# Performance work log

Hardware: AMD Instinct MI355X
Metric: run time of the kernel (lower is better)

The kernel has to match this reference:

```python
import jax, jax.numpy as jnp
import numpy as np

V = 1_000_000   # num_embeddings
D = 64          # embedding_dim
B = 16_384      # number of bags (batch)
L = 50          # history length per bag


def setup_inputs() -> dict:
    key = jax.random.key(0)
    k_w, k_i = jax.random.split(key)
    weight = jax.random.normal(k_w, (V, D), dtype=jnp.float32) * 0.01
    indices = jax.random.randint(k_i, (B * L,), 0, V, dtype=jnp.int64)
    # bag start offsets (uniform bags of length L, starting at 0, sorted)
    offsets = (jnp.arange(B, dtype=jnp.int64) * L)
    return {"indices": indices, "offsets": offsets, "weight": weight}


def reference(indices, offsets, weight):
    """embedding_bag(indices, weight, offsets, mode='mean').

    indices: [T] int flat ids into weight rows
    offsets: [B] int bag start positions into indices (sorted, offsets[0]==0)
    weight:  [V, D] float embedding table
    returns: [B, D] per-bag mean of gathered embeddings
    """
    T = indices.shape[0]
    num_bags = offsets.shape[0]
    # bag id for each flat index position
    seg = jnp.searchsorted(offsets, jnp.arange(T), side="right") - 1  # [T]
    gathered = weight[indices]                                        # [T, D]
    sums = jax.ops.segment_sum(gathered, seg, num_segments=num_bags)  # [B, D]
    counts = jax.ops.segment_sum(
        jnp.ones((T,), dtype=weight.dtype), seg, num_segments=num_bags
    )                                                                 # [B]
    return sums / jnp.maximum(counts, 1.0)[:, None]
```

## Files before the change

kernel.cpp:

```cpp
#include <hip/hip_runtime.h>


__global__ __launch_bounds__(256) void FreqAwareEmbedding_kernel(
    const int* __restrict__ indices,
    const int* __restrict__ offsets,
    const float4* __restrict__ weight4,
    float4* __restrict__ out4,
    int B, int T)
{
    const int wave = (int)((blockIdx.x * blockDim.x + threadIdx.x) >> 6);
    if (wave >= B) return;
    const int lane = threadIdx.x & 63;
    const int sub  = lane >> 4;
    const int col  = lane & 15;

    const int start = offsets[wave];
    const int end   = (wave + 1 < B) ? offsets[wave + 1] : T;
    const int count = end - start;

    float4 acc = make_float4(0.f, 0.f, 0.f, 0.f);

    if (count <= 64) {
        int myidx = 0;
        if (lane < count) myidx = indices[start + lane];

        #pragma unroll
        for (int t = 0; t < 16; ++t) {
            const int j  = sub + 4 * t;
            const int jj = (j < count) ? j : 0;
            const int idx = __shfl(myidx, jj, 64);
            if (j < count) {
                const float4 v = weight4[(size_t)idx * 16 + col];
                acc.x += v.x; acc.y += v.y; acc.z += v.z; acc.w += v.w;
            }
        }
    } else {
        for (int j = sub; j < count; j += 4) {
            const int idx = indices[start + j];
            const float4 v = weight4[(size_t)idx * 16 + col];
            acc.x += v.x; acc.y += v.y; acc.z += v.z; acc.w += v.w;
        }
    }

    #pragma unroll
    for (int m = 16; m <= 32; m <<= 1) {
        acc.x += __shfl_xor(acc.x, m, 64);
        acc.y += __shfl_xor(acc.y, m, 64);
        acc.z += __shfl_xor(acc.z, m, 64);
        acc.w += __shfl_xor(acc.w, m, 64);
    }

    const float inv = 1.0f / (float)((count > 0) ? count : 1);
    acc.x *= inv; acc.y *= inv; acc.z *= inv; acc.w *= inv;

    if (sub == 0) {
        out4[(size_t)wave * 16 + col] = acc;
    }
}

extern "C" void kernel_launch(void* const* d_in, const int* in_sizes, int n_in,
                              void* d_out, int out_size, void* d_ws, size_t ws_size,
                              hipStream_t stream) {
    const int*   indices = (const int*)d_in[0];
    const int*   offsets = (const int*)d_in[1];
    const float* weight  = (const float*)d_in[2];

    const int T = in_sizes[0];
    const int B = in_sizes[1];

    const int bags_per_block = 4;
    const int grid = (B + bags_per_block - 1) / bags_per_block;

    FreqAwareEmbedding_kernel<<<grid, 256, 0, stream>>>(
        indices, offsets, (const float4*)weight, (float4*)d_out, B, T);
}
```

Measured before the change: 326.3 us.

## Assign one bag per 16-lane group and stage indices in shared memory

```diff
diff --git a/kernel.cpp b/kernel.cpp
--- a/kernel.cpp
+++ b/kernel.cpp
@@ -1,5 +1,8 @@
 #include <hip/hip_runtime.h>
 
+
+constexpr int kBagsPerBlock = 16;
+constexpr int kMaxFast = 64;
 
 __global__ __launch_bounds__(256) void FreqAwareEmbedding_kernel(
     const int* __restrict__ indices,
@@ -8,53 +11,57 @@
     float4* __restrict__ out4,
     int B, int T)
 {
-    const int wave = (int)((blockIdx.x * blockDim.x + threadIdx.x) >> 6);
-    if (wave >= B) return;
-    const int lane = threadIdx.x & 63;
-    const int sub  = lane >> 4;
-    const int col  = lane & 15;
+    __shared__ int sidx[kBagsPerBlock][kMaxFast + 1];
 
-    const int start = offsets[wave];
-    const int end   = (wave + 1 < B) ? offsets[wave + 1] : T;
-    const int count = end - start;
+    const int tid = threadIdx.x;
+    const int grp = tid >> 4;
+    const int col = tid & 15;
+    const int bag = blockIdx.x * kBagsPerBlock + grp;
+
+    int start = 0, count = 0;
+    if (bag < B) {
+        start = offsets[bag];
+        const int end = (bag + 1 < B) ? offsets[bag + 1] : T;
+        count = end - start;
+    }
+
+    const bool fast = (count <= kMaxFast);
+    if (fast) {
+        for (int j = col; j < count; j += 16)
+            sidx[grp][j] = indices[start + j];
+    }
+    __syncthreads();
 
     float4 acc = make_float4(0.f, 0.f, 0.f, 0.f);
 
-    if (count <= 64) {
-        int myidx = 0;
-        if (lane < count) myidx = indices[start + lane];
-
-        #pragma unroll
-        for (int t = 0; t < 16; ++t) {
-            const int j  = sub + 4 * t;
-            const int jj = (j < count) ? j : 0;
-            const int idx = __shfl(myidx, jj, 64);
-            if (j < count) {
-                const float4 v = weight4[(size_t)idx * 16 + col];
+    if (fast) {
+        const int* sp = sidx[grp];
+        int j = 0;
+        for (; j + 10 <= count; j += 10) {
+            int id[10];
+            #pragma unroll
+            for (int u = 0; u < 10; ++u) id[u] = sp[j + u];
+            #pragma unroll
+            for (int u = 0; u < 10; ++u) {
+                const float4 v = weight4[(size_t)id[u] * 16 + col];
                 acc.x += v.x; acc.y += v.y; acc.z += v.z; acc.w += v.w;
             }
         }
-    } else {
-        for (int j = sub; j < count; j += 4) {
-            const int idx = indices[start + j];
-            const float4 v = weight4[(size_t)idx * 16 + col];
+        for (; j < count; ++j) {
+            const float4 v = weight4[(size_t)sp[j] * 16 + col];
+            acc.x += v.x; acc.y += v.y; acc.z += v.z; acc.w += v.w;
+        }
+    } else if (count > 0) {
+        for (int j = 0; j < count; ++j) {
+            const float4 v = weight4[(size_t)indices[start + j] * 16 + col];
             acc.x += v.x; acc.y += v.y; acc.z += v.z; acc.w += v.w;
         }
     }
 
-    #pragma unroll
-    for (int m = 16; m <= 32; m <<= 1) {
-        acc.x += __shfl_xor(acc.x, m, 64);
-        acc.y += __shfl_xor(acc.y, m, 64);
-        acc.z += __shfl_xor(acc.z, m, 64);
-        acc.w += __shfl_xor(acc.w, m, 64);
-    }
-
-    const float inv = 1.0f / (float)((count > 0) ? count : 1);
-    acc.x *= inv; acc.y *= inv; acc.z *= inv; acc.w *= inv;
-
-    if (sub == 0) {
-        out4[(size_t)wave * 16 + col] = acc;
+    if (bag < B) {
+        const float inv = 1.0f / (float)((count > 0) ? count : 1);
+        acc.x *= inv; acc.y *= inv; acc.z *= inv; acc.w *= inv;
+        out4[(size_t)bag * 16 + col] = acc;
     }
 }
 
@@ -68,8 +75,7 @@
     const int T = in_sizes[0];
     const int B = in_sizes[1];
 
-    const int bags_per_block = 4;
-    const int grid = (B + bags_per_block - 1) / bags_per_block;
+    const int grid = (B + kBagsPerBlock - 1) / kBagsPerBlock;
 
     FreqAwareEmbedding_kernel<<<grid, 256, 0, stream>>>(
         indices, offsets, (const float4*)weight, (float4*)d_out, B, T);
```

Measured after the change: 324.9 us, median of 2. No clear change (-0.4%).
